# Performance work log

Measured on AMD Instinct MI355X. Metric: run time of the kernel, lower is better.

The kernel has to match this reference:

```python
import jax, jax.numpy as jnp
import numpy as np


def setup_inputs() -> dict:
    key = jax.random.key(0)
    k1, k2, k3, k4 = jax.random.split(key, 4)
    N, IN, OUT, R, B = 8192, 256, 256, 8, 4
    a = jax.random.normal(k1, (N, N), dtype=jnp.float32)
    x = jax.random.normal(k2, (N, IN, R), dtype=jnp.float32)
    w_bases = jax.random.normal(k3, (B, IN, OUT), dtype=jnp.float32) * (1.0 / np.sqrt(IN))
    w_rel = jax.random.normal(k4, (R, B), dtype=jnp.float32) * 0.5
    return {"a": a, "x": x, "w_bases": w_bases, "w_rel": w_rel}


def reference(a, x, w_bases, w_rel):
    # Basis-combined per-relation weights: [R, IN, OUT]
    w = jnp.einsum('rb,bio->rio', w_rel, w_bases)
    # Per-relation aggregation: support_r = a @ x[:, :, r] -> stack as [N, R, IN]
    # (matches torch.cat([a @ x[:,:,r] for r], dim=1) ordering)
    supports = jnp.einsum('nm,mir->nri', a, x)  # [N, R, IN]
    # tmp [N, R*IN] @ weights [R*IN, OUT] fused as one einsum
    out = jnp.einsum('nri,rio->no', supports, w)  # [N, OUT]
    return out
```

## Files before the change

### kernel.cpp

```cpp
#include <hip/hip_runtime.h>
#include <hip/hip_bf16.h>
#include <stdint.h>

typedef __fp16 f16x2 __attribute__((ext_vector_type(2)));
typedef __fp16 f16x8 __attribute__((ext_vector_type(8)));
typedef float  f32x4 __attribute__((ext_vector_type(4)));

#define GLOBAL_AS __attribute__((address_space(1)))
#define LDS_AS    __attribute__((address_space(3)))

#define NN   8192
#define INC  256
#define OUTC 256
#define K2   2048
#define YTN  ((size_t)OUTC * NN)

__device__ __forceinline__ void async_copy16(const void* g, void* l) {
    __builtin_amdgcn_global_load_lds((const GLOBAL_AS uint32_t*)g,
                                     (LDS_AS uint32_t*)l, 16, 0, 0);
}

__global__ void build_w2t16(const float* __restrict__ wb, const float* __restrict__ wr,
                            __fp16* __restrict__ W2T16) {
    int o = blockIdx.x;
    int i = threadIdx.x;
    float s[8];
#pragma unroll
    for (int r = 0; r < 8; ++r) s[r] = 0.f;
#pragma unroll
    for (int b = 0; b < 4; ++b) {
        float w = wb[((size_t)((b << 8) + i)) * OUTC + o];
#pragma unroll
        for (int r = 0; r < 8; ++r) s[r] = fmaf(wr[r * 4 + b], w, s[r]);
    }
    f16x8 out;
    f16x2* p = (f16x2*)&out;
    p[0] = __builtin_amdgcn_cvt_pkrtz(s[0], s[1]);
    p[1] = __builtin_amdgcn_cvt_pkrtz(s[2], s[3]);
    p[2] = __builtin_amdgcn_cvt_pkrtz(s[4], s[5]);
    p[3] = __builtin_amdgcn_cvt_pkrtz(s[6], s[7]);
    *reinterpret_cast<f16x8*>(&W2T16[(size_t)o * K2 + i * 8]) = out;
}

constexpr int BM = 128, BN = 128, BK = 32;

template <bool AF32, bool BF32>
__global__ __launch_bounds__(256, 2)
void gemm_mixed(const void* __restrict__ Ap, const void* __restrict__ Bp,
                float* __restrict__ Cp, int M, int N, int K, int kPerSplit) {
    constexpr int ABYTES = BM * BK * (AF32 ? 4 : 2);
    constexpr int BBYTES = BN * BK * (BF32 ? 4 : 2);
    __shared__ __align__(16) char smem[ABYTES + BBYTES];
    char* As = smem;
    char* Bs = smem + ABYTES;

    const int bm = blockIdx.x * BM;
    const int bn = blockIdx.y * BN;
    const int k0 = blockIdx.z * kPerSplit;

    const int tid  = threadIdx.x;
    const int lane = tid & 63;
    const int wave = tid >> 6;
    const int wm   = (wave >> 1) * 64;
    const int wn   = (wave & 1) * 64;
    const int quad = lane >> 4;
    const int l16  = lane & 15;

    f32x4 acc[4][4];
#pragma unroll
    for (int ti = 0; ti < 4; ++ti)
#pragma unroll
        for (int tj = 0; tj < 4; ++tj)
            acc[ti][tj] = (f32x4){0.f, 0.f, 0.f, 0.f};

    for (int kc = k0; kc < k0 + kPerSplit; kc += BK) {
        if (AF32) {
            const float* Ag = (const float*)Ap;
#pragma unroll
            for (int i = 0; i < 4; ++i) {
                int r0 = wave * 32 + i * 8;
                const float* g = Ag + (size_t)(bm + r0 + (lane >> 3)) * K + kc + ((lane & 7) << 2);
                async_copy16(g, As + (size_t)r0 * BK * 4);
            }
        } else {
            const __fp16* Ag = (const __fp16*)Ap;
#pragma unroll
            for (int i = 0; i < 2; ++i) {
                int r0 = wave * 32 + i * 16;
                const __fp16* g = Ag + (size_t)(bm + r0 + (lane >> 2)) * K + kc + ((lane & 3) << 3);
                async_copy16(g, As + (size_t)r0 * BK * 2);
            }
        }
        if (BF32) {
            const float* Bg = (const float*)Bp;
#pragma unroll
            for (int i = 0; i < 4; ++i) {
                int r0 = wave * 32 + i * 8;
                const float* g = Bg + (size_t)(bn + r0 + (lane >> 3)) * K + kc + ((lane & 7) << 2);
                async_copy16(g, Bs + (size_t)r0 * BK * 4);
            }
        } else {
            const __fp16* Bg = (const __fp16*)Bp;
#pragma unroll
            for (int i = 0; i < 2; ++i) {
                int r0 = wave * 32 + i * 16;
                const __fp16* g = Bg + (size_t)(bn + r0 + (lane >> 2)) * K + kc + ((lane & 3) << 3);
                async_copy16(g, Bs + (size_t)r0 * BK * 2);
            }
        }
        __syncthreads();

        f16x8 af[4], bf[4];
#pragma unroll
        for (int t = 0; t < 4; ++t) {
            if (AF32) {
                const float* Ar = (const float*)As + (size_t)(wm + t * 16 + l16) * BK + quad * 8;
                f32x4 u0 = *(const f32x4*)Ar;
                f32x4 u1 = *(const f32x4*)(Ar + 4);
                f16x2* p = (f16x2*)&af[t];
                p[0] = __builtin_amdgcn_cvt_pkrtz(u0[0], u0[1]);
                p[1] = __builtin_amdgcn_cvt_pkrtz(u0[2], u0[3]);
                p[2] = __builtin_amdgcn_cvt_pkrtz(u1[0], u1[1]);
                p[3] = __builtin_amdgcn_cvt_pkrtz(u1[2], u1[3]);
            } else {
                af[t] = *(const f16x8*)((const __fp16*)As + (size_t)(wm + t * 16 + l16) * BK + quad * 8);
            }
            if (BF32) {
                const float* Br = (const float*)Bs + (size_t)(wn + t * 16 + l16) * BK + quad * 8;
                f32x4 u0 = *(const f32x4*)Br;
                f32x4 u1 = *(const f32x4*)(Br + 4);
                f16x2* p = (f16x2*)&bf[t];
                p[0] = __builtin_amdgcn_cvt_pkrtz(u0[0], u0[1]);
                p[1] = __builtin_amdgcn_cvt_pkrtz(u0[2], u0[3]);
                p[2] = __builtin_amdgcn_cvt_pkrtz(u1[0], u1[1]);
                p[3] = __builtin_amdgcn_cvt_pkrtz(u1[2], u1[3]);
            } else {
                bf[t] = *(const f16x8*)((const __fp16*)Bs + (size_t)(wn + t * 16 + l16) * BK + quad * 8);
            }
        }
#pragma unroll
        for (int ti = 0; ti < 4; ++ti)
#pragma unroll
            for (int tj = 0; tj < 4; ++tj)
                acc[ti][tj] = __builtin_amdgcn_mfma_f32_16x16x32_f16(
                    af[ti], bf[tj], acc[ti][tj], 0, 0, 0);
        __syncthreads();
    }

    float* Cz = Cp + (size_t)blockIdx.z * M * N;
#pragma unroll
    for (int ti = 0; ti < 4; ++ti)
#pragma unroll
        for (int tj = 0; tj < 4; ++tj)
#pragma unroll
            for (int r = 0; r < 4; ++r) {
                int row = bm + wm + ti * 16 + quad * 4 + r;
                int col = bn + wn + tj * 16 + l16;
                Cz[(size_t)row * N + col] = acc[ti][tj][r];
            }
}

constexpr int BM2 = 128, BN2 = 256, BK2 = 32;

__global__ __launch_bounds__(256, 2)
void gemm2_wide(const float* __restrict__ Ap, const __fp16* __restrict__ Bp,
                float* __restrict__ Cp, int M, int K, int kPerSplit) {
    __shared__ __align__(16) char smem[BM2 * BK2 * 4 + BN2 * BK2 * 2];
    char* As = smem;
    char* Bs = smem + BM2 * BK2 * 4;

    const int bm = blockIdx.x * BM2;
    const int k0 = blockIdx.z * kPerSplit;

    const int tid  = threadIdx.x;
    const int lane = tid & 63;
    const int wave = tid >> 6;
    const int wm   = (wave >> 1) * 64;
    const int wn   = (wave & 1) * 128;
    const int quad = lane >> 4;
    const int l16  = lane & 15;

    f32x4 acc[4][8];
#pragma unroll
    for (int ti = 0; ti < 4; ++ti)
#pragma unroll
        for (int tj = 0; tj < 8; ++tj)
            acc[ti][tj] = (f32x4){0.f, 0.f, 0.f, 0.f};

    for (int kc = k0; kc < k0 + kPerSplit; kc += BK2) {
#pragma unroll
        for (int i = 0; i < 4; ++i) {
            int r0 = wave * 32 + i * 8;
            const float* g = Ap + (size_t)(bm + r0 + (lane >> 3)) * K + kc + ((lane & 7) << 2);
            async_copy16(g, As + (size_t)r0 * BK2 * 4);
        }
#pragma unroll
        for (int i = 0; i < 4; ++i) {
            int r0 = wave * 64 + i * 16;
            const __fp16* g = Bp + (size_t)(r0 + (lane >> 2)) * K + kc + ((lane & 3) << 3);
            async_copy16(g, Bs + (size_t)r0 * BK2 * 2);
        }
        __syncthreads();

        f16x8 af[4], bf[8];
#pragma unroll
        for (int t = 0; t < 4; ++t) {
            const float* Ar = (const float*)As + (size_t)(wm + t * 16 + l16) * BK2 + quad * 8;
            f32x4 u0 = *(const f32x4*)Ar;
            f32x4 u1 = *(const f32x4*)(Ar + 4);
            f16x2* p = (f16x2*)&af[t];
            p[0] = __builtin_amdgcn_cvt_pkrtz(u0[0], u0[1]);
            p[1] = __builtin_amdgcn_cvt_pkrtz(u0[2], u0[3]);
            p[2] = __builtin_amdgcn_cvt_pkrtz(u1[0], u1[1]);
            p[3] = __builtin_amdgcn_cvt_pkrtz(u1[2], u1[3]);
        }
#pragma unroll
        for (int t = 0; t < 8; ++t)
            bf[t] = *(const f16x8*)((const __fp16*)Bs + (size_t)(wn + t * 16 + l16) * BK2 + quad * 8);

#pragma unroll
        for (int ti = 0; ti < 4; ++ti)
#pragma unroll
            for (int tj = 0; tj < 8; ++tj)
                acc[ti][tj] = __builtin_amdgcn_mfma_f32_16x16x32_f16(
                    af[ti], bf[tj], acc[ti][tj], 0, 0, 0);
        __syncthreads();
    }

    float* Cz = Cp + (size_t)blockIdx.z * M * BN2;
#pragma unroll
    for (int ti = 0; ti < 4; ++ti)
#pragma unroll
        for (int tj = 0; tj < 8; ++tj)
#pragma unroll
            for (int r = 0; r < 4; ++r) {
                int row = bm + wm + ti * 16 + quad * 4 + r;
                int col = wn + tj * 16 + l16;
                Cz[(size_t)row * BN2 + col] = acc[ti][tj][r];
            }
}

__global__ void reduce_yT(const float* __restrict__ yTp, __fp16* __restrict__ yT16) {
    size_t base = ((size_t)blockIdx.x * 256 + threadIdx.x) * 8;
    f32x4 s0 = (f32x4){0.f, 0.f, 0.f, 0.f};
    f32x4 s1 = (f32x4){0.f, 0.f, 0.f, 0.f};
#pragma unroll
    for (int z = 0; z < 4; ++z) {
        const float* p = yTp + (size_t)z * YTN + base;
        s0 += *(const f32x4*)p;
        s1 += *(const f32x4*)(p + 4);
    }
    f16x8 out;
    f16x2* p = (f16x2*)&out;
    p[0] = __builtin_amdgcn_cvt_pkrtz(s0[0], s0[1]);
    p[1] = __builtin_amdgcn_cvt_pkrtz(s0[2], s0[3]);
    p[2] = __builtin_amdgcn_cvt_pkrtz(s1[0], s1[1]);
    p[3] = __builtin_amdgcn_cvt_pkrtz(s1[2], s1[3]);
    *reinterpret_cast<f16x8*>(&yT16[base]) = out;
}

__global__ void reduce_out(const float* __restrict__ op, float* __restrict__ out) {
    size_t base = ((size_t)blockIdx.x * 256 + threadIdx.x) * 4;
    f32x4 s = (f32x4){0.f, 0.f, 0.f, 0.f};
#pragma unroll
    for (int z = 0; z < 8; ++z)
        s += *(const f32x4*)(op + (size_t)z * YTN + base);
    *reinterpret_cast<f32x4*>(&out[base]) = s;
}

extern "C" void kernel_launch(void* const* d_in, const int* in_sizes, int n_in,
                              void* d_out, int out_size, void* d_ws, size_t ws_size,
                              hipStream_t stream) {
    const float* a  = (const float*)d_in[0];
    const float* x  = (const float*)d_in[1];
    const float* wb = (const float*)d_in[2];
    const float* wr = (const float*)d_in[3];
    float* out = (float*)d_out;

    char* w = (char*)d_ws;
    float*  yT_p  = (float*)(w);
    __fp16* yT16  = (__fp16*)(w + ((size_t)32 << 20));
    float*  out_p = (float*)(w + ((size_t)36 << 20));
    __fp16* W2T16 = (__fp16*)(w + ((size_t)100 << 20));

    build_w2t16<<<dim3(256), dim3(256), 0, stream>>>(wb, wr, W2T16);

    gemm_mixed<false, true><<<dim3(2, 64, 4), dim3(256), 0, stream>>>(
        W2T16, x, yT_p, 256, NN, K2, 512);

    reduce_yT<<<dim3(1024), dim3(256), 0, stream>>>(yT_p, yT16);

    gemm2_wide<<<dim3(64, 1, 8), dim3(256), 0, stream>>>(
        a, yT16, out_p, NN, NN, 1024);

    reduce_out<<<dim3(2048), dim3(256), 0, stream>>>(out_p, out);
}
```

Measured before the change: 470.0 us.

## Stream fp32 operand from global into registers and double-buffer swizzled fp16 LDS tile

Both GEMMs now load their fp32 operand (x in GEMM1, the adjacency matrix a in GEMM2) straight from global memory into registers and convert it to fp16 there, instead of staging it through LDS. Only the fp16 operand is kept in LDS, double-buffered and prefetched one tile ahead, so each iteration needs one barrier instead of two. The LDS layout uses an XOR swizzle to reduce bank conflicts. The catch is that the direct global loads are not coalesced across the whole tile and have to be hidden by the MFMA work in the same iteration.

After: 546.2 us. +16.2%, slower.

```diff
diff --git a/kernel.cpp b/kernel.cpp
--- a/kernel.cpp
+++ b/kernel.cpp
@@ -1,5 +1,4 @@
 #include <hip/hip_runtime.h>
-#include <hip/hip_bf16.h>
 #include <stdint.h>
 
 typedef __fp16 f16x2 __attribute__((ext_vector_type(2)));
@@ -18,6 +17,16 @@
 __device__ __forceinline__ void async_copy16(const void* g, void* l) {
     __builtin_amdgcn_global_load_lds((const GLOBAL_AS uint32_t*)g,
                                      (LDS_AS uint32_t*)l, 16, 0, 0);
+}
+
+__device__ __forceinline__ f16x8 cvt_f32x8_to_f16x8(f32x4 u0, f32x4 u1) {
+    f16x8 out;
+    f16x2* p = (f16x2*)&out;
+    p[0] = __builtin_amdgcn_cvt_pkrtz(u0[0], u0[1]);
+    p[1] = __builtin_amdgcn_cvt_pkrtz(u0[2], u0[3]);
+    p[2] = __builtin_amdgcn_cvt_pkrtz(u1[0], u1[1]);
+    p[3] = __builtin_amdgcn_cvt_pkrtz(u1[2], u1[3]);
+    return out;
 }
 
 __global__ void build_w2t16(const float* __restrict__ wb, const float* __restrict__ wr,
@@ -42,20 +51,12 @@
     *reinterpret_cast<f16x8*>(&W2T16[(size_t)o * K2 + i * 8]) = out;
 }
 
-constexpr int BM = 128, BN = 128, BK = 32;
-
-template <bool AF32, bool BF32>
 __global__ __launch_bounds__(256, 2)
-void gemm_mixed(const void* __restrict__ Ap, const void* __restrict__ Bp,
-                float* __restrict__ Cp, int M, int N, int K, int kPerSplit) {
-    constexpr int ABYTES = BM * BK * (AF32 ? 4 : 2);
-    constexpr int BBYTES = BN * BK * (BF32 ? 4 : 2);
-    __shared__ __align__(16) char smem[ABYTES + BBYTES];
-    char* As = smem;
-    char* Bs = smem + ABYTES;
-
-    const int bm = blockIdx.x * BM;
-    const int bn = blockIdx.y * BN;
+void gemm1_xstream(const __fp16* __restrict__ W2, const float* __restrict__ X,
+                   float* __restrict__ Cp, int kPerSplit) {
+    __shared__ __align__(16) __fp16 As[2][128 * 32];
+    const int bm = blockIdx.x * 128;
+    const int bn = blockIdx.y * 128;
     const int k0 = blockIdx.z * kPerSplit;
 
     const int tid  = threadIdx.x;
@@ -73,70 +74,49 @@
         for (int tj = 0; tj < 4; ++tj)
             acc[ti][tj] = (f32x4){0.f, 0.f, 0.f, 0.f};
 
-    for (int kc = k0; kc < k0 + kPerSplit; kc += BK) {
-        if (AF32) {
-            const float* Ag = (const float*)Ap;
-#pragma unroll
-            for (int i = 0; i < 4; ++i) {
-                int r0 = wave * 32 + i * 8;
-                const float* g = Ag + (size_t)(bm + r0 + (lane >> 3)) * K + kc + ((lane & 7) << 2);
-                async_copy16(g, As + (size_t)r0 * BK * 4);
-            }
-        } else {
-            const __fp16* Ag = (const __fp16*)Ap;
+    const int nt = kPerSplit / 32;
+    int cur = 0;
+
+    {
+#pragma unroll
+        for (int i = 0; i < 2; ++i) {
+            int r0 = wave * 32 + i * 16;
+            int r  = r0 + (lane >> 2);
+            int c  = (lane & 3) ^ ((r >> 1) & 3);
+            async_copy16(W2 + (size_t)(bm + r) * K2 + k0 + c * 8,
+                         (char*)As[0] + r0 * 64);
+        }
+    }
+
+    for (int t = 0; t < nt; ++t) {
+        __syncthreads();
+        if (t + 1 < nt) {
+            int kc = k0 + (t + 1) * 32;
 #pragma unroll
             for (int i = 0; i < 2; ++i) {
                 int r0 = wave * 32 + i * 16;
-                const __fp16* g = Ag + (size_t)(bm + r0 + (lane >> 2)) * K + kc + ((lane & 3) << 3);
-                async_copy16(g, As + (size_t)r0 * BK * 2);
-            }
-        }
-        if (BF32) {
-            const float* Bg = (const float*)Bp;
-#pragma unroll
-            for (int i = 0; i < 4; ++i) {
-                int r0 = wave * 32 + i * 8;
-                const float* g = Bg + (size_t)(bn + r0 + (lane >> 3)) * K + kc + ((lane & 7) << 2);
-                async_copy16(g, Bs + (size_t)r0 * BK * 4);
-            }
-        } else {
-            const __fp16* Bg = (const __fp16*)Bp;
-#pragma unroll
-            for (int i = 0; i < 2; ++i) {
-                int r0 = wave * 32 + i * 16;
-                const __fp16* g = Bg + (size_t)(bn + r0 + (lane >> 2)) * K + kc + ((lane & 3) << 3);
-                async_copy16(g, Bs + (size_t)r0 * BK * 2);
-            }
-        }
-        __syncthreads();
-
-        f16x8 af[4], bf[4];
-#pragma unroll
-        for (int t = 0; t < 4; ++t) {
-            if (AF32) {
-                const float* Ar = (const float*)As + (size_t)(wm + t * 16 + l16) * BK + quad * 8;
-                f32x4 u0 = *(const f32x4*)Ar;
-                f32x4 u1 = *(const f32x4*)(Ar + 4);
-                f16x2* p = (f16x2*)&af[t];
-                p[0] = __builtin_amdgcn_cvt_pkrtz(u0[0], u0[1]);
-                p[1] = __builtin_amdgcn_cvt_pkrtz(u0[2], u0[3]);
-                p[2] = __builtin_amdgcn_cvt_pkrtz(u1[0], u1[1]);
-                p[3] = __builtin_amdgcn_cvt_pkrtz(u1[2], u1[3]);
-            } else {
-                af[t] = *(const f16x8*)((const __fp16*)As + (size_t)(wm + t * 16 + l16) * BK + quad * 8);
-            }
-            if (BF32) {
-                const float* Br = (const float*)Bs + (size_t)(wn + t * 16 + l16) * BK + quad * 8;
-                f32x4 u0 = *(const f32x4*)Br;
-                f32x4 u1 = *(const f32x4*)(Br + 4);
-                f16x2* p = (f16x2*)&bf[t];
-                p[0] = __builtin_amdgcn_cvt_pkrtz(u0[0], u0[1]);
-                p[1] = __builtin_amdgcn_cvt_pkrtz(u0[2], u0[3]);
-                p[2] = __builtin_amdgcn_cvt_pkrtz(u1[0], u1[1]);
-                p[3] = __builtin_amdgcn_cvt_pkrtz(u1[2], u1[3]);
-            } else {
-                bf[t] = *(const f16x8*)((const __fp16*)Bs + (size_t)(wn + t * 16 + l16) * BK + quad * 8);
-            }
+                int r  = r0 + (lane >> 2);
+                int c  = (lane & 3) ^ ((r >> 1) & 3);
+                async_copy16(W2 + (size_t)(bm + r) * K2 + kc + c * 8,
+                             (char*)As[cur ^ 1] + r0 * 64);
+            }
+        }
+        const int kc = k0 + t * 32;
+
+        f16x8 bf[4];
+#pragma unroll
+        for (int j = 0; j < 4; ++j) {
+            const float* g = X + (size_t)(bn + wn + j * 16 + l16) * K2 + kc + quad * 8;
+            f32x4 u0 = *(const f32x4*)g;
+            f32x4 u1 = *(const f32x4*)(g + 4);
+            bf[j] = cvt_f32x8_to_f16x8(u0, u1);
+        }
+        f16x8 af[4];
+#pragma unroll
+        for (int j = 0; j < 4; ++j) {
+            int row = wm + j * 16 + l16;
+            int p   = quad ^ ((row >> 1) & 3);
+            af[j] = *(const f16x8*)(&As[cur][0] + row * 32 + p * 8);
         }
 #pragma unroll
         for (int ti = 0; ti < 4; ++ti)
@@ -144,10 +124,10 @@
             for (int tj = 0; tj < 4; ++tj)
                 acc[ti][tj] = __builtin_amdgcn_mfma_f32_16x16x32_f16(
                     af[ti], bf[tj], acc[ti][tj], 0, 0, 0);
-        __syncthreads();
-    }
-
-    float* Cz = Cp + (size_t)blockIdx.z * M * N;
+        cur ^= 1;
+    }
+
+    float* Cz = Cp + (size_t)blockIdx.z * 256 * NN;
 #pragma unroll
     for (int ti = 0; ti < 4; ++ti)
 #pragma unroll
@@ -156,20 +136,15 @@
             for (int r = 0; r < 4; ++r) {
                 int row = bm + wm + ti * 16 + quad * 4 + r;
                 int col = bn + wn + tj * 16 + l16;
-                Cz[(size_t)row * N + col] = acc[ti][tj][r];
-            }
-}
-
-constexpr int BM2 = 128, BN2 = 256, BK2 = 32;
+                Cz[(size_t)row * NN + col] = acc[ti][tj][r];
+            }
+}
 
 __global__ __launch_bounds__(256, 2)
-void gemm2_wide(const float* __restrict__ Ap, const __fp16* __restrict__ Bp,
-                float* __restrict__ Cp, int M, int K, int kPerSplit) {
-    __shared__ __align__(16) char smem[BM2 * BK2 * 4 + BN2 * BK2 * 2];
-    char* As = smem;
-    char* Bs = smem + BM2 * BK2 * 4;
-
-    const int bm = blockIdx.x * BM2;
+void gemm2_astream(const float* __restrict__ A, const __fp16* __restrict__ Y,
+                   float* __restrict__ Cp, int kPerSplit) {
+    __shared__ __align__(16) __fp16 Bs[2][256 * 32];
+    const int bm = blockIdx.x * 128;
     const int k0 = blockIdx.z * kPerSplit;
 
     const int tid  = threadIdx.x;
@@ -187,47 +162,60 @@
         for (int tj = 0; tj < 8; ++tj)
             acc[ti][tj] = (f32x4){0.f, 0.f, 0.f, 0.f};
 
-    for (int kc = k0; kc < k0 + kPerSplit; kc += BK2) {
-#pragma unroll
-        for (int i = 0; i < 4; ++i) {
-            int r0 = wave * 32 + i * 8;
-            const float* g = Ap + (size_t)(bm + r0 + (lane >> 3)) * K + kc + ((lane & 7) << 2);
-            async_copy16(g, As + (size_t)r0 * BK2 * 4);
-        }
+    const int nt = kPerSplit / 32;
+    int cur = 0;
+
+    {
 #pragma unroll
         for (int i = 0; i < 4; ++i) {
             int r0 = wave * 64 + i * 16;
-            const __fp16* g = Bp + (size_t)(r0 + (lane >> 2)) * K + kc + ((lane & 3) << 3);
-            async_copy16(g, Bs + (size_t)r0 * BK2 * 2);
-        }
+            int r  = r0 + (lane >> 2);
+            int c  = (lane & 3) ^ ((r >> 1) & 3);
+            async_copy16(Y + (size_t)r * NN + k0 + c * 8,
+                         (char*)Bs[0] + r0 * 64);
+        }
+    }
+
+    for (int t = 0; t < nt; ++t) {
         __syncthreads();
-
-        f16x8 af[4], bf[8];
-#pragma unroll
-        for (int t = 0; t < 4; ++t) {
-            const float* Ar = (const float*)As + (size_t)(wm + t * 16 + l16) * BK2 + quad * 8;
-            f32x4 u0 = *(const f32x4*)Ar;
-            f32x4 u1 = *(const f32x4*)(Ar + 4);
-            f16x2* p = (f16x2*)&af[t];
-            p[0] = __builtin_amdgcn_cvt_pkrtz(u0[0], u0[1]);
-            p[1] = __builtin_amdgcn_cvt_pkrtz(u0[2], u0[3]);
-            p[2] = __builtin_amdgcn_cvt_pkrtz(u1[0], u1[1]);
-            p[3] = __builtin_amdgcn_cvt_pkrtz(u1[2], u1[3]);
-        }
-#pragma unroll
-        for (int t = 0; t < 8; ++t)
-            bf[t] = *(const f16x8*)((const __fp16*)Bs + (size_t)(wn + t * 16 + l16) * BK2 + quad * 8);
-
+        if (t + 1 < nt) {
+            int kc = k0 + (t + 1) * 32;
+#pragma unroll
+            for (int i = 0; i < 4; ++i) {
+                int r0 = wave * 64 + i * 16;
+                int r  = r0 + (lane >> 2);
+                int c  = (lane & 3) ^ ((r >> 1) & 3);
+                async_copy16(Y + (size_t)r * NN + kc + c * 8,
+                             (char*)Bs[cur ^ 1] + r0 * 64);
+            }
+        }
+        const int kc = k0 + t * 32;
+
+        f16x8 af[4];
+#pragma unroll
+        for (int j = 0; j < 4; ++j) {
+            const float* g = A + (size_t)(bm + wm + j * 16 + l16) * NN + kc + quad * 8;
+            f32x4 u0 = *(const f32x4*)g;
+            f32x4 u1 = *(const f32x4*)(g + 4);
+            af[j] = cvt_f32x8_to_f16x8(u0, u1);
+        }
+        f16x8 bf[8];
+#pragma unroll
+        for (int j = 0; j < 8; ++j) {
+            int row = wn + j * 16 + l16;
+            int p   = quad ^ ((row >> 1) & 3);
+            bf[j] = *(const f16x8*)(&Bs[cur][0] + row * 32 + p * 8);
+        }
 #pragma unroll
         for (int ti = 0; ti < 4; ++ti)
 #pragma unroll
             for (int tj = 0; tj < 8; ++tj)
                 acc[ti][tj] = __builtin_amdgcn_mfma_f32_16x16x32_f16(
                     af[ti], bf[tj], acc[ti][tj], 0, 0, 0);
-        __syncthreads();
-    }
-
-    float* Cz = Cp + (size_t)blockIdx.z * M * BN2;
+        cur ^= 1;
+    }
+
+    float* Cz = Cp + (size_t)blockIdx.z * NN * 256;
 #pragma unroll
     for (int ti = 0; ti < 4; ++ti)
 #pragma unroll
@@ -236,7 +224,7 @@
             for (int r = 0; r < 4; ++r) {
                 int row = bm + wm + ti * 16 + quad * 4 + r;
                 int col = wn + tj * 16 + l16;
-                Cz[(size_t)row * BN2 + col] = acc[ti][tj][r];
+                Cz[(size_t)row * 256 + col] = acc[ti][tj][r];
             }
 }
 
@@ -250,13 +238,7 @@
         s0 += *(const f32x4*)p;
         s1 += *(const f32x4*)(p + 4);
     }
-    f16x8 out;
-    f16x2* p = (f16x2*)&out;
-    p[0] = __builtin_amdgcn_cvt_pkrtz(s0[0], s0[1]);
-    p[1] = __builtin_amdgcn_cvt_pkrtz(s0[2], s0[3]);
-    p[2] = __builtin_amdgcn_cvt_pkrtz(s1[0], s1[1]);
-    p[3] = __builtin_amdgcn_cvt_pkrtz(s1[2], s1[3]);
-    *reinterpret_cast<f16x8*>(&yT16[base]) = out;
+    *reinterpret_cast<f16x8*>(&yT16[base]) = cvt_f32x8_to_f16x8(s0, s1);
 }
 
 __global__ void reduce_out(const float* __restrict__ op, float* __restrict__ out) {
@@ -285,13 +267,11 @@
 
     build_w2t16<<<dim3(256), dim3(256), 0, stream>>>(wb, wr, W2T16);
 
-    gemm_mixed<false, true><<<dim3(2, 64, 4), dim3(256), 0, stream>>>(
-        W2T16, x, yT_p, 256, NN, K2, 512);
+    gemm1_xstream<<<dim3(2, 64, 4), dim3(256), 0, stream>>>(W2T16, x, yT_p, 512);
 
     reduce_yT<<<dim3(1024), dim3(256), 0, stream>>>(yT_p, yT16);
 
-    gemm2_wide<<<dim3(64, 1, 8), dim3(256), 0, stream>>>(
-        a, yT16, out_p, NN, NN, 1024);
+    gemm2_astream<<<dim3(64, 1, 8), dim3(256), 0, stream>>>(a, yT16, out_p, 1024);
 
     reduce_out<<<dim3(2048), dim3(256), 0, stream>>>(out_p, out);
 }
```
